# Optimization experiments

Measured on AMD Instinct MI355X. Metric: run time of the kernel, lower is better.

## Reference

```python
import jax, jax.numpy as jnp
import numpy as np

N_NODES = 50000
N_EDGES = 800000
HIDDEN = 128


def setup_inputs() -> dict:
    key = jax.random.key(0)
    ks = jax.random.split(key, 8)
    z = jax.random.normal(ks[0], (N_NODES, HIDDEN), dtype=jnp.float32)
    weights = jax.random.normal(ks[1], (N_EDGES, 1), dtype=jnp.float32)
    sources = jax.random.randint(ks[2], (N_EDGES,), 0, N_NODES)
    dests = jax.random.randint(ks[3], (N_EDGES,), 0, N_NODES)
    # Linear params (stored [in, out]); scale ~ 1/sqrt(fan_in) like torch default
    in_m = 2 * HIDDEN + 1
    in_u = 2 * HIDDEN
    Wm = jax.random.uniform(ks[4], (in_m, HIDDEN), dtype=jnp.float32, minval=-1.0, maxval=1.0) / np.sqrt(in_m)
    bm = jax.random.uniform(ks[5], (HIDDEN,), dtype=jnp.float32, minval=-1.0, maxval=1.0) / np.sqrt(in_m)
    Wu = jax.random.uniform(ks[6], (in_u, HIDDEN), dtype=jnp.float32, minval=-1.0, maxval=1.0) / np.sqrt(in_u)
    bu = jax.random.uniform(ks[7], (HIDDEN,), dtype=jnp.float32, minval=-1.0, maxval=1.0) / np.sqrt(in_u)
    return {"z": z, "weights": weights, "sources": sources, "dests": dests,
            "Wm": Wm, "bm": bm, "Wu": Wu, "bu": bu}


def reference(z, weights, sources, dests, Wm, bm, Wu, bu):
    n = z.shape[0]
    # gather + concat message input: [E, 2d+1]
    inp = jnp.concatenate([z[dests], z[sources], weights], axis=1)
    messages = inp @ Wm + bm                      # [E, d]
    # scatter_reduce amax over destination nodes; empty segments -> -inf
    m = jax.ops.segment_max(messages, dests, num_segments=n)
    m = jnp.where(jnp.isneginf(m), jnp.zeros_like(m), m)
    h = jnp.concatenate([z, m], axis=1) @ Wu + bu  # [N, d]
    return h
```

## Files before the change

kernel.cpp:

```cpp
#include <hip/hip_runtime.h>
#include <math.h>

#define HIDDEN 128
#define PAD_DEG 64
#define NPART 8
#define CHUNK 4096
#define CNT_STRIDE 16
#define NSCATTER_BLOCKS 256
#define XCC_GETREG_IMM 63508

typedef __attribute__((ext_vector_type(8))) _Float16 f16x8;
typedef __attribute__((ext_vector_type(4))) float f32x4;
typedef __attribute__((ext_vector_type(2))) _Float16 h2;

__device__ inline unsigned short f2h(float x) {
    _Float16 h = (_Float16)x;
    return __builtin_bit_cast(unsigned short, h);
}
__device__ inline float h2f(unsigned short u) {
    return (float)__builtin_bit_cast(_Float16, u);
}
__device__ inline float h2f_lo(unsigned int u) { return h2f((unsigned short)(u & 0xffff)); }
__device__ inline float h2f_hi(unsigned int u) { return h2f((unsigned short)(u >> 16)); }
__device__ inline h2 hmax2(h2 a, h2 b) {
    h2 r;
    r[0] = a[0] > b[0] ? a[0] : b[0];
    r[1] = a[1] > b[1] ? a[1] : b[1];
    return r;
}

__global__ void prep_kernel(const float* __restrict__ Wm, const float* __restrict__ Wu,
                            unsigned short* __restrict__ WmT0, unsigned short* __restrict__ WmT1,
                            unsigned short* __restrict__ WuT, float* __restrict__ wlast,
                            int* __restrict__ counts, int* __restrict__ tick, int n) {
    int t = blockIdx.x * blockDim.x + threadIdx.x;
    if (t < 16384) {
        int nn = t >> 7, k = t & 127;
        WmT0[t] = f2h(Wm[k * 128 + nn]);
    } else if (t < 32768) {
        int s = t - 16384;
        int nn = s >> 7, k = s & 127;
        WmT1[s] = f2h(Wm[(128 + k) * 128 + nn]);
    } else if (t < 65536) {
        int s = t - 32768;
        int nn = s >> 8, k = s & 255;
        WuT[s] = f2h(Wu[k * 128 + nn]);
    } else if (t < 65664) {
        int i = t - 65536;
        wlast[i] = Wm[256 * 128 + i];
    } else if (t < 65664 + 4 * n) {
        ((int4*)counts)[t - 65664] = make_int4(0, 0, 0, 0);
    } else if (t < 65664 + 4 * n + 128) {
        tick[t - 65664 - 4 * n] = 0;
    }
}

__global__ __launch_bounds__(256) void fused_sg(const int* __restrict__ dests,
                                                const int* __restrict__ sources,
                                                const float* __restrict__ weights,
                                                int* __restrict__ counts,
                                                int* __restrict__ tick,
                                                unsigned int* __restrict__ edge_pk,
                                                int E, int span, int n, int nchunks,
                                                const float* __restrict__ Z,
                                                const unsigned short* __restrict__ WmT0,
                                                const unsigned short* __restrict__ WmT1,
                                                unsigned short* __restrict__ P1h,
                                                unsigned short* __restrict__ P2h,
                                                int nscatter) {
    __shared__ unsigned short As[64][136];
    __shared__ unsigned short Bs[128][136];
    __shared__ int s_chunk;

    if (blockIdx.x < nscatter) {
        const int xcd = (int)(__builtin_amdgcn_s_getreg(XCC_GETREG_IMM) & 7);
        const int lo = xcd * span;
        const int hi = min(lo + span, n);

        for (int it = 0; it <= nchunks; ++it) {
            if (threadIdx.x == 0) {
                s_chunk = __hip_atomic_fetch_add(&tick[xcd * 16], 1,
                                                 __ATOMIC_RELAXED, __HIP_MEMORY_SCOPE_AGENT);
            }
            __syncthreads();
            const int chunk = s_chunk;
            __syncthreads();
            if (chunk >= nchunks || chunk < 0) break;

            const int base = chunk * CHUNK + threadIdx.x * 4;
            int dd[16];
            unsigned int pk[16];
            int pos[16];

#pragma unroll
            for (int g = 0; g < 4; ++g) {
                int e = base + g * 1024;
                if (e + 3 < E) {
                    int4 dq = *(const int4*)&dests[e];
                    int4 sq = *(const int4*)&sources[e];
                    float4 wq = *(const float4*)&weights[e];
                    dd[g * 4 + 0] = dq.x; dd[g * 4 + 1] = dq.y;
                    dd[g * 4 + 2] = dq.z; dd[g * 4 + 3] = dq.w;
                    pk[g * 4 + 0] = (unsigned int)(sq.x & 0xffff) | ((unsigned int)f2h(wq.x) << 16);
                    pk[g * 4 + 1] = (unsigned int)(sq.y & 0xffff) | ((unsigned int)f2h(wq.y) << 16);
                    pk[g * 4 + 2] = (unsigned int)(sq.z & 0xffff) | ((unsigned int)f2h(wq.z) << 16);
                    pk[g * 4 + 3] = (unsigned int)(sq.w & 0xffff) | ((unsigned int)f2h(wq.w) << 16);
                } else {
#pragma unroll
                    for (int j = 0; j < 4; ++j) {
                        int ej = e + j;
                        if (ej < E) {
                            dd[g * 4 + j] = dests[ej];
                            pk[g * 4 + j] = (unsigned int)(sources[ej] & 0xffff) |
                                            ((unsigned int)f2h(weights[ej]) << 16);
                        } else {
                            dd[g * 4 + j] = -1;
                            pk[g * 4 + j] = 0;
                        }
                    }
                }
            }

#pragma unroll
            for (int k = 0; k < 16; ++k) {
                bool act = (dd[k] >= lo) && (dd[k] < hi);
                pos[k] = act ? atomicAdd(&counts[(size_t)dd[k] * CNT_STRIDE], 1) : PAD_DEG;
            }

#pragma unroll
            for (int k = 0; k < 16; ++k) {
                if (pos[k] < PAD_DEG) {
                    edge_pk[(size_t)dd[k] * PAD_DEG + pos[k]] = pk[k];
                }
            }
        }
        return;
    }

    const int m0 = (blockIdx.x - nscatter) * 64;
    const int tid = threadIdx.x;
    const int wave = tid >> 6, lane = tid & 63;
    const int l15 = lane & 15, q = lane >> 4;
    const int wrow = wave * 16;

#pragma unroll
    for (int i = 0; i < 4; ++i) {
        int f = tid + i * 256;
        int row = f >> 4, c8 = f & 15;
        int gr = min(m0 + row, n - 1);
        const float4* src = (const float4*)&Z[(size_t)gr * 128 + c8 * 8];
        float4 a = src[0], b = src[1];
        f16x8 hv;
        hv[0] = (_Float16)a.x; hv[1] = (_Float16)a.y; hv[2] = (_Float16)a.z; hv[3] = (_Float16)a.w;
        hv[4] = (_Float16)b.x; hv[5] = (_Float16)b.y; hv[6] = (_Float16)b.z; hv[7] = (_Float16)b.w;
        *(f16x8*)&As[row][c8 * 8] = hv;
    }

    for (int part = 0; part < 2; ++part) {
        const float4* bsrc = (const float4*)(part == 0 ? WmT0 : WmT1);
        unsigned short* Out = part == 0 ? P1h : P2h;

#pragma unroll
        for (int i = 0; i < 8; ++i) {
            int f = tid + i * 256;
            int row = f >> 4, c4 = f & 15;
            *(float4*)&Bs[row][c4 * 8] = bsrc[row * 16 + c4];
        }
        __syncthreads();

        f32x4 acc[8];
#pragma unroll
        for (int nt = 0; nt < 8; ++nt) acc[nt] = (f32x4){0.f, 0.f, 0.f, 0.f};

#pragma unroll
        for (int ks = 0; ks < 4; ++ks) {
            int k0 = ks * 32;
            f16x8 a = *(const f16x8*)&As[wrow + l15][k0 + q * 8];
#pragma unroll
            for (int nt = 0; nt < 8; ++nt) {
                f16x8 b = *(const f16x8*)&Bs[nt * 16 + l15][k0 + q * 8];
                acc[nt] = __builtin_amdgcn_mfma_f32_16x16x32_f16(a, b, acc[nt], 0, 0, 0);
            }
        }

#pragma unroll
        for (int nt = 0; nt < 8; ++nt) {
#pragma unroll
            for (int r = 0; r < 4; ++r) {
                int row = m0 + wrow + q * 4 + r;
                if (row < n) Out[(size_t)row * 128 + nt * 16 + l15] = f2h(acc[nt][r]);
            }
        }
        __syncthreads();
    }
}

__global__ __launch_bounds__(256) void segmax_kernel(const unsigned short* __restrict__ P1h,
                                                     const unsigned short* __restrict__ P2h,
                                                     const int* __restrict__ counts,
                                                     const unsigned int* __restrict__ edge_pk,
                                                     const float* __restrict__ wlast,
                                                     const float* __restrict__ bm,
                                                     unsigned short* __restrict__ Mh, int n) {
    const int wave = threadIdx.x >> 6;
    const int lane = threadIdx.x & 63;
    const int v = blockIdx.x * 4 + wave;
    if (v >= n) return;

    const int l16 = lane & 15;
    const int e4 = lane >> 4;
    const uint4* P2q = (const uint4*)P2h;
    const int cnt = min(counts[(size_t)v * CNT_STRIDE], PAD_DEG);

    int pk = (lane < cnt) ? (int)edge_pk[(size_t)v * PAD_DEG + lane] : 0;

    uint4 p1 = make_uint4(0, 0, 0, 0);
    if (e4 == 0 && cnt > 0) p1 = ((const uint4*)P1h)[(size_t)v * 16 + l16];

    float4 wfa = ((const float4*)wlast)[l16 * 2];
    float4 wfb = ((const float4*)wlast)[l16 * 2 + 1];
    h2 wl0, wl1, wl2, wl3;
    wl0[0] = (_Float16)wfa.x; wl0[1] = (_Float16)wfa.y;
    wl1[0] = (_Float16)wfa.z; wl1[1] = (_Float16)wfa.w;
    wl2[0] = (_Float16)wfb.x; wl2[1] = (_Float16)wfb.y;
    wl3[0] = (_Float16)wfb.z; wl3[1] = (_Float16)wfb.w;

    const h2 NEGINF = __builtin_bit_cast(h2, 0xFC00FC00u);
    h2 a0 = NEGINF, a1 = NEGINF, a2 = NEGINF, a3 = NEGINF;

    int j = 0;
    for (; j + 16 <= cnt; j += 16) {
        unsigned int pa = (unsigned int)__shfl(pk, j + e4);
        unsigned int pb = (unsigned int)__shfl(pk, j + 4 + e4);
        unsigned int pc = (unsigned int)__shfl(pk, j + 8 + e4);
        unsigned int pd = (unsigned int)__shfl(pk, j + 12 + e4);
        uint4 ua = P2q[(size_t)(pa & 0xffff) * 16 + l16];
        uint4 ub = P2q[(size_t)(pb & 0xffff) * 16 + l16];
        uint4 uc = P2q[(size_t)(pc & 0xffff) * 16 + l16];
        uint4 ud = P2q[(size_t)(pd & 0xffff) * 16 + l16];
        h2 wva = __builtin_bit_cast(h2, (pa & 0xffff0000u) | (pa >> 16));
        h2 wvb = __builtin_bit_cast(h2, (pb & 0xffff0000u) | (pb >> 16));
        h2 wvc = __builtin_bit_cast(h2, (pc & 0xffff0000u) | (pc >> 16));
        h2 wvd = __builtin_bit_cast(h2, (pd & 0xffff0000u) | (pd >> 16));
        a0 = hmax2(a0, wva * wl0 + __builtin_bit_cast(h2, ua.x));
        a1 = hmax2(a1, wva * wl1 + __builtin_bit_cast(h2, ua.y));
        a2 = hmax2(a2, wva * wl2 + __builtin_bit_cast(h2, ua.z));
        a3 = hmax2(a3, wva * wl3 + __builtin_bit_cast(h2, ua.w));
        a0 = hmax2(a0, wvb * wl0 + __builtin_bit_cast(h2, ub.x));
        a1 = hmax2(a1, wvb * wl1 + __builtin_bit_cast(h2, ub.y));
        a2 = hmax2(a2, wvb * wl2 + __builtin_bit_cast(h2, ub.z));
        a3 = hmax2(a3, wvb * wl3 + __builtin_bit_cast(h2, ub.w));
        a0 = hmax2(a0, wvc * wl0 + __builtin_bit_cast(h2, uc.x));
        a1 = hmax2(a1, wvc * wl1 + __builtin_bit_cast(h2, uc.y));
        a2 = hmax2(a2, wvc * wl2 + __builtin_bit_cast(h2, uc.z));
        a3 = hmax2(a3, wvc * wl3 + __builtin_bit_cast(h2, uc.w));
        a0 = hmax2(a0, wvd * wl0 + __builtin_bit_cast(h2, ud.x));
        a1 = hmax2(a1, wvd * wl1 + __builtin_bit_cast(h2, ud.y));
        a2 = hmax2(a2, wvd * wl2 + __builtin_bit_cast(h2, ud.z));
        a3 = hmax2(a3, wvd * wl3 + __builtin_bit_cast(h2, ud.w));
    }
    for (; j + 8 <= cnt; j += 8) {
        unsigned int pa = (unsigned int)__shfl(pk, j + e4);
        unsigned int pb = (unsigned int)__shfl(pk, j + 4 + e4);
        uint4 ua = P2q[(size_t)(pa & 0xffff) * 16 + l16];
        uint4 ub = P2q[(size_t)(pb & 0xffff) * 16 + l16];
        h2 wva = __builtin_bit_cast(h2, (pa & 0xffff0000u) | (pa >> 16));
        h2 wvb = __builtin_bit_cast(h2, (pb & 0xffff0000u) | (pb >> 16));
        a0 = hmax2(a0, wva * wl0 + __builtin_bit_cast(h2, ua.x));
        a1 = hmax2(a1, wva * wl1 + __builtin_bit_cast(h2, ua.y));
        a2 = hmax2(a2, wva * wl2 + __builtin_bit_cast(h2, ua.z));
        a3 = hmax2(a3, wva * wl3 + __builtin_bit_cast(h2, ua.w));
        a0 = hmax2(a0, wvb * wl0 + __builtin_bit_cast(h2, ub.x));
        a1 = hmax2(a1, wvb * wl1 + __builtin_bit_cast(h2, ub.y));
        a2 = hmax2(a2, wvb * wl2 + __builtin_bit_cast(h2, ub.z));
        a3 = hmax2(a3, wvb * wl3 + __builtin_bit_cast(h2, ub.w));
    }
    for (; j < cnt; j += 4) {
        int idx = j + e4;
        bool valid = idx < cnt;
        unsigned int pa = (unsigned int)__shfl(pk, valid ? idx : 0);
        if (valid) {
            uint4 ua = P2q[(size_t)(pa & 0xffff) * 16 + l16];
            h2 wva = __builtin_bit_cast(h2, (pa & 0xffff0000u) | (pa >> 16));
            a0 = hmax2(a0, wva * wl0 + __builtin_bit_cast(h2, ua.x));
            a1 = hmax2(a1, wva * wl1 + __builtin_bit_cast(h2, ua.y));
            a2 = hmax2(a2, wva * wl2 + __builtin_bit_cast(h2, ua.z));
            a3 = hmax2(a3, wva * wl3 + __builtin_bit_cast(h2, ua.w));
        }
    }

    a0 = hmax2(a0, __builtin_bit_cast(h2, __shfl_xor(__builtin_bit_cast(int, a0), 16)));
    a1 = hmax2(a1, __builtin_bit_cast(h2, __shfl_xor(__builtin_bit_cast(int, a1), 16)));
    a2 = hmax2(a2, __builtin_bit_cast(h2, __shfl_xor(__builtin_bit_cast(int, a2), 16)));
    a3 = hmax2(a3, __builtin_bit_cast(h2, __shfl_xor(__builtin_bit_cast(int, a3), 16)));
    a0 = hmax2(a0, __builtin_bit_cast(h2, __shfl_xor(__builtin_bit_cast(int, a0), 32)));
    a1 = hmax2(a1, __builtin_bit_cast(h2, __shfl_xor(__builtin_bit_cast(int, a1), 32)));
    a2 = hmax2(a2, __builtin_bit_cast(h2, __shfl_xor(__builtin_bit_cast(int, a2), 32)));
    a3 = hmax2(a3, __builtin_bit_cast(h2, __shfl_xor(__builtin_bit_cast(int, a3), 32)));

    if (e4 == 0) {
        uint4 o = make_uint4(0, 0, 0, 0);
        if (cnt > 0) {
            float4 b0 = ((const float4*)bm)[l16 * 2];
            float4 b1 = ((const float4*)bm)[l16 * 2 + 1];
            float m0 = h2f_lo(p1.x) + b0.x + (float)a0[0];
            float m1 = h2f_hi(p1.x) + b0.y + (float)a0[1];
            float m2 = h2f_lo(p1.y) + b0.z + (float)a1[0];
            float m3 = h2f_hi(p1.y) + b0.w + (float)a1[1];
            float m4 = h2f_lo(p1.z) + b1.x + (float)a2[0];
            float m5 = h2f_hi(p1.z) + b1.y + (float)a2[1];
            float m6 = h2f_lo(p1.w) + b1.z + (float)a3[0];
            float m7 = h2f_hi(p1.w) + b1.w + (float)a3[1];
            o.x = (unsigned int)f2h(m0) | ((unsigned int)f2h(m1) << 16);
            o.y = (unsigned int)f2h(m2) | ((unsigned int)f2h(m3) << 16);
            o.z = (unsigned int)f2h(m4) | ((unsigned int)f2h(m5) << 16);
            o.w = (unsigned int)f2h(m6) | ((unsigned int)f2h(m7) << 16);
        } else {
            unsigned int zh = (unsigned int)f2h(0.f);
            unsigned int zz = zh | (zh << 16);
            o = make_uint4(zz, zz, zz, zz);
        }
        ((uint4*)Mh)[(size_t)v * 16 + l16] = o;
    }
}

__global__ __launch_bounds__(256) void gemm_out(const float* __restrict__ Z,
                                                const unsigned short* __restrict__ Mh,
                                                const unsigned short* __restrict__ WuT,
                                                const float* __restrict__ bu,
                                                float* __restrict__ H, int n) {
    __shared__ unsigned short As[64][136];
    __shared__ unsigned short Bs[128][136];

    const int m0 = blockIdx.x * 64;
    const int tid = threadIdx.x;
    const int wave = tid >> 6, lane = tid & 63;
    const int l15 = lane & 15, q = lane >> 4;
    const int wrow = wave * 16;

    f32x4 acc[8];
#pragma unroll
    for (int nt = 0; nt < 8; ++nt) acc[nt] = (f32x4){0.f, 0.f, 0.f, 0.f};

    for (int h = 0; h < 2; ++h) {
#pragma unroll
        for (int i = 0; i < 8; ++i) {
            int f = tid + i * 256;
            int row = f >> 4, c4 = f & 15;
            *(float4*)&Bs[row][c4 * 8] = ((const float4*)WuT)[row * 32 + h * 16 + c4];
        }
        if (h == 0) {
#pragma unroll
            for (int i = 0; i < 4; ++i) {
                int f = tid + i * 256;
                int row = f >> 4, c8 = f & 15;
                int gr = min(m0 + row, n - 1);
                const float4* src = (const float4*)&Z[(size_t)gr * 128 + c8 * 8];
                float4 a = src[0], b = src[1];
                f16x8 hv;
                hv[0] = (_Float16)a.x; hv[1] = (_Float16)a.y; hv[2] = (_Float16)a.z; hv[3] = (_Float16)a.w;
                hv[4] = (_Float16)b.x; hv[5] = (_Float16)b.y; hv[6] = (_Float16)b.z; hv[7] = (_Float16)b.w;
                *(f16x8*)&As[row][c8 * 8] = hv;
            }
        } else {
#pragma unroll
            for (int i = 0; i < 4; ++i) {
                int f = tid + i * 256;
                int row = f >> 4, c4 = f & 15;
                int gr = min(m0 + row, n - 1);
                *(float4*)&As[row][c4 * 8] = ((const float4*)&Mh[(size_t)gr * 128])[c4];
            }
        }
        __syncthreads();

#pragma unroll
        for (int ks = 0; ks < 4; ++ks) {
            int k0 = ks * 32;
            f16x8 a = *(const f16x8*)&As[wrow + l15][k0 + q * 8];
#pragma unroll
            for (int nt = 0; nt < 8; ++nt) {
                f16x8 b = *(const f16x8*)&Bs[nt * 16 + l15][k0 + q * 8];
                acc[nt] = __builtin_amdgcn_mfma_f32_16x16x32_f16(a, b, acc[nt], 0, 0, 0);
            }
        }
        __syncthreads();
    }

#pragma unroll
    for (int nt = 0; nt < 8; ++nt) {
        int col = nt * 16 + l15;
        float bias = bu[col];
#pragma unroll
        for (int r = 0; r < 4; ++r) {
            int row = m0 + wrow + q * 4 + r;
            if (row < n) H[(size_t)row * 128 + col] = acc[nt][r] + bias;
        }
    }
}

extern "C" void kernel_launch(void* const* d_in, const int* in_sizes, int n_in,
                              void* d_out, int out_size, void* d_ws, size_t ws_size,
                              hipStream_t stream) {
    const float* z = (const float*)d_in[0];
    const float* weights = (const float*)d_in[1];
    const int* sources = (const int*)d_in[2];
    const int* dests = (const int*)d_in[3];
    const float* Wm = (const float*)d_in[4];
    const float* bm = (const float*)d_in[5];
    const float* Wu = (const float*)d_in[6];
    const float* bu = (const float*)d_in[7];

    const int n = in_sizes[0] / HIDDEN;
    const int E = in_sizes[1];
    float* H = (float*)d_out;

    char* w = (char*)d_ws;
    auto alloc = [&](size_t bytes) { void* p = w; w += (bytes + 255) & ~(size_t)255; return p; };
    unsigned short* P1h = (unsigned short*)alloc((size_t)n * 128 * 2);
    unsigned short* Mh  = (unsigned short*)alloc((size_t)n * 128 * 2);
    unsigned short* WmT0 = (unsigned short*)alloc(16384 * 2);
    unsigned short* WmT1 = (unsigned short*)alloc(16384 * 2);
    unsigned short* WuT  = (unsigned short*)alloc(32768 * 2);
    float* wlast = (float*)alloc(128 * 4);
    int* counts  = (int*)alloc((size_t)n * CNT_STRIDE * 4);
    int* tick    = (int*)alloc(128 * 4);
    unsigned int* edge_pk = (unsigned int*)alloc((size_t)n * PAD_DEG * 4);

    unsigned short* P2h = (unsigned short*)d_out;

    const int mblocks = (n + 63) / 64;
    const int prep_threads = 65664 + 4 * n + 128;
    const int span = (n + NPART - 1) / NPART;
    const int nchunks = (E + CHUNK - 1) / CHUNK;
    const int nscatter = NSCATTER_BLOCKS;

    prep_kernel<<<(prep_threads + 255) / 256, 256, 0, stream>>>(Wm, Wu, WmT0, WmT1, WuT,
                                                                wlast, counts, tick, n);
    fused_sg<<<nscatter + mblocks, 256, 0, stream>>>(dests, sources, weights, counts, tick,
                                                     edge_pk, E, span, n, nchunks,
                                                     z, WmT0, WmT1, P1h, P2h, nscatter);
    segmax_kernel<<<(n + 3) / 4, 256, 0, stream>>>(P1h, P2h, counts, edge_pk,
                                                   wlast, bm, Mh, n);
    gemm_out<<<mblocks, 256, 0, stream>>>(z, Mh, WuT, bu, H, n);
}
```

Measured before the change: 184.6 us.

## Fuse segment-max into output GEMM, building the message tile in shared memory

Merges the segment-max kernel into the final GEMM. Each wave computes the max-aggregated messages for its 16 rows and writes them straight into the shared-memory A tile, removing the intermediate Mh buffer and one kernel launch. P2h moves from the output buffer to the workspace because the fused kernel writes H while other blocks may still read P2h. The trade-off is much lower parallelism for the latency-bound gather phase: each wave now handles 16 nodes sequentially instead of one, with only a one-node prefetch of edge indices.

```diff
diff --git a/kernel.cpp b/kernel.cpp
--- a/kernel.cpp
+++ b/kernel.cpp
@@ -195,140 +195,16 @@
     }
 }
 
-__global__ __launch_bounds__(256) void segmax_kernel(const unsigned short* __restrict__ P1h,
-                                                     const unsigned short* __restrict__ P2h,
-                                                     const int* __restrict__ counts,
-                                                     const unsigned int* __restrict__ edge_pk,
-                                                     const float* __restrict__ wlast,
-                                                     const float* __restrict__ bm,
-                                                     unsigned short* __restrict__ Mh, int n) {
-    const int wave = threadIdx.x >> 6;
-    const int lane = threadIdx.x & 63;
-    const int v = blockIdx.x * 4 + wave;
-    if (v >= n) return;
-
-    const int l16 = lane & 15;
-    const int e4 = lane >> 4;
-    const uint4* P2q = (const uint4*)P2h;
-    const int cnt = min(counts[(size_t)v * CNT_STRIDE], PAD_DEG);
-
-    int pk = (lane < cnt) ? (int)edge_pk[(size_t)v * PAD_DEG + lane] : 0;
-
-    uint4 p1 = make_uint4(0, 0, 0, 0);
-    if (e4 == 0 && cnt > 0) p1 = ((const uint4*)P1h)[(size_t)v * 16 + l16];
-
-    float4 wfa = ((const float4*)wlast)[l16 * 2];
-    float4 wfb = ((const float4*)wlast)[l16 * 2 + 1];
-    h2 wl0, wl1, wl2, wl3;
-    wl0[0] = (_Float16)wfa.x; wl0[1] = (_Float16)wfa.y;
-    wl1[0] = (_Float16)wfa.z; wl1[1] = (_Float16)wfa.w;
-    wl2[0] = (_Float16)wfb.x; wl2[1] = (_Float16)wfb.y;
-    wl3[0] = (_Float16)wfb.z; wl3[1] = (_Float16)wfb.w;
-
-    const h2 NEGINF = __builtin_bit_cast(h2, 0xFC00FC00u);
-    h2 a0 = NEGINF, a1 = NEGINF, a2 = NEGINF, a3 = NEGINF;
-
-    int j = 0;
-    for (; j + 16 <= cnt; j += 16) {
-        unsigned int pa = (unsigned int)__shfl(pk, j + e4);
-        unsigned int pb = (unsigned int)__shfl(pk, j + 4 + e4);
-        unsigned int pc = (unsigned int)__shfl(pk, j + 8 + e4);
-        unsigned int pd = (unsigned int)__shfl(pk, j + 12 + e4);
-        uint4 ua = P2q[(size_t)(pa & 0xffff) * 16 + l16];
-        uint4 ub = P2q[(size_t)(pb & 0xffff) * 16 + l16];
-        uint4 uc = P2q[(size_t)(pc & 0xffff) * 16 + l16];
-        uint4 ud = P2q[(size_t)(pd & 0xffff) * 16 + l16];
-        h2 wva = __builtin_bit_cast(h2, (pa & 0xffff0000u) | (pa >> 16));
-        h2 wvb = __builtin_bit_cast(h2, (pb & 0xffff0000u) | (pb >> 16));
-        h2 wvc = __builtin_bit_cast(h2, (pc & 0xffff0000u) | (pc >> 16));
-        h2 wvd = __builtin_bit_cast(h2, (pd & 0xffff0000u) | (pd >> 16));
-        a0 = hmax2(a0, wva * wl0 + __builtin_bit_cast(h2, ua.x));
-        a1 = hmax2(a1, wva * wl1 + __builtin_bit_cast(h2, ua.y));
-        a2 = hmax2(a2, wva * wl2 + __builtin_bit_cast(h2, ua.z));
-        a3 = hmax2(a3, wva * wl3 + __builtin_bit_cast(h2, ua.w));
-        a0 = hmax2(a0, wvb * wl0 + __builtin_bit_cast(h2, ub.x));
-        a1 = hmax2(a1, wvb * wl1 + __builtin_bit_cast(h2, ub.y));
-        a2 = hmax2(a2, wvb * wl2 + __builtin_bit_cast(h2, ub.z));
-        a3 = hmax2(a3, wvb * wl3 + __builtin_bit_cast(h2, ub.w));
-        a0 = hmax2(a0, wvc * wl0 + __builtin_bit_cast(h2, uc.x));
-        a1 = hmax2(a1, wvc * wl1 + __builtin_bit_cast(h2, uc.y));
-        a2 = hmax2(a2, wvc * wl2 + __builtin_bit_cast(h2, uc.z));
-        a3 = hmax2(a3, wvc * wl3 + __builtin_bit_cast(h2, uc.w));
-        a0 = hmax2(a0, wvd * wl0 + __builtin_bit_cast(h2, ud.x));
-        a1 = hmax2(a1, wvd * wl1 + __builtin_bit_cast(h2, ud.y));
-        a2 = hmax2(a2, wvd * wl2 + __builtin_bit_cast(h2, ud.z));
-        a3 = hmax2(a3, wvd * wl3 + __builtin_bit_cast(h2, ud.w));
-    }
-    for (; j + 8 <= cnt; j += 8) {
-        unsigned int pa = (unsigned int)__shfl(pk, j + e4);
-        unsigned int pb = (unsigned int)__shfl(pk, j + 4 + e4);
-        uint4 ua = P2q[(size_t)(pa & 0xffff) * 16 + l16];
-        uint4 ub = P2q[(size_t)(pb & 0xffff) * 16 + l16];
-        h2 wva = __builtin_bit_cast(h2, (pa & 0xffff0000u) | (pa >> 16));
-        h2 wvb = __builtin_bit_cast(h2, (pb & 0xffff0000u) | (pb >> 16));
-        a0 = hmax2(a0, wva * wl0 + __builtin_bit_cast(h2, ua.x));
-        a1 = hmax2(a1, wva * wl1 + __builtin_bit_cast(h2, ua.y));
-        a2 = hmax2(a2, wva * wl2 + __builtin_bit_cast(h2, ua.z));
-        a3 = hmax2(a3, wva * wl3 + __builtin_bit_cast(h2, ua.w));
-        a0 = hmax2(a0, wvb * wl0 + __builtin_bit_cast(h2, ub.x));
-        a1 = hmax2(a1, wvb * wl1 + __builtin_bit_cast(h2, ub.y));
-        a2 = hmax2(a2, wvb * wl2 + __builtin_bit_cast(h2, ub.z));
-        a3 = hmax2(a3, wvb * wl3 + __builtin_bit_cast(h2, ub.w));
-    }
-    for (; j < cnt; j += 4) {
-        int idx = j + e4;
-        bool valid = idx < cnt;
-        unsigned int pa = (unsigned int)__shfl(pk, valid ? idx : 0);
-        if (valid) {
-            uint4 ua = P2q[(size_t)(pa & 0xffff) * 16 + l16];
-            h2 wva = __builtin_bit_cast(h2, (pa & 0xffff0000u) | (pa >> 16));
-            a0 = hmax2(a0, wva * wl0 + __builtin_bit_cast(h2, ua.x));
-            a1 = hmax2(a1, wva * wl1 + __builtin_bit_cast(h2, ua.y));
-            a2 = hmax2(a2, wva * wl2 + __builtin_bit_cast(h2, ua.z));
-            a3 = hmax2(a3, wva * wl3 + __builtin_bit_cast(h2, ua.w));
-        }
-    }
-
-    a0 = hmax2(a0, __builtin_bit_cast(h2, __shfl_xor(__builtin_bit_cast(int, a0), 16)));
-    a1 = hmax2(a1, __builtin_bit_cast(h2, __shfl_xor(__builtin_bit_cast(int, a1), 16)));
-    a2 = hmax2(a2, __builtin_bit_cast(h2, __shfl_xor(__builtin_bit_cast(int, a2), 16)));
-    a3 = hmax2(a3, __builtin_bit_cast(h2, __shfl_xor(__builtin_bit_cast(int, a3), 16)));
-    a0 = hmax2(a0, __builtin_bit_cast(h2, __shfl_xor(__builtin_bit_cast(int, a0), 32)));
-    a1 = hmax2(a1, __builtin_bit_cast(h2, __shfl_xor(__builtin_bit_cast(int, a1), 32)));
-    a2 = hmax2(a2, __builtin_bit_cast(h2, __shfl_xor(__builtin_bit_cast(int, a2), 32)));
-    a3 = hmax2(a3, __builtin_bit_cast(h2, __shfl_xor(__builtin_bit_cast(int, a3), 32)));
-
-    if (e4 == 0) {
-        uint4 o = make_uint4(0, 0, 0, 0);
-        if (cnt > 0) {
-            float4 b0 = ((const float4*)bm)[l16 * 2];
-            float4 b1 = ((const float4*)bm)[l16 * 2 + 1];
-            float m0 = h2f_lo(p1.x) + b0.x + (float)a0[0];
-            float m1 = h2f_hi(p1.x) + b0.y + (float)a0[1];
-            float m2 = h2f_lo(p1.y) + b0.z + (float)a1[0];
-            float m3 = h2f_hi(p1.y) + b0.w + (float)a1[1];
-            float m4 = h2f_lo(p1.z) + b1.x + (float)a2[0];
-            float m5 = h2f_hi(p1.z) + b1.y + (float)a2[1];
-            float m6 = h2f_lo(p1.w) + b1.z + (float)a3[0];
-            float m7 = h2f_hi(p1.w) + b1.w + (float)a3[1];
-            o.x = (unsigned int)f2h(m0) | ((unsigned int)f2h(m1) << 16);
-            o.y = (unsigned int)f2h(m2) | ((unsigned int)f2h(m3) << 16);
-            o.z = (unsigned int)f2h(m4) | ((unsigned int)f2h(m5) << 16);
-            o.w = (unsigned int)f2h(m6) | ((unsigned int)f2h(m7) << 16);
-        } else {
-            unsigned int zh = (unsigned int)f2h(0.f);
-            unsigned int zz = zh | (zh << 16);
-            o = make_uint4(zz, zz, zz, zz);
-        }
-        ((uint4*)Mh)[(size_t)v * 16 + l16] = o;
-    }
-}
-
-__global__ __launch_bounds__(256) void gemm_out(const float* __restrict__ Z,
-                                                const unsigned short* __restrict__ Mh,
-                                                const unsigned short* __restrict__ WuT,
-                                                const float* __restrict__ bu,
-                                                float* __restrict__ H, int n) {
+__global__ __launch_bounds__(256) void segmax_gemm(const float* __restrict__ Z,
+                                                   const unsigned short* __restrict__ P1h,
+                                                   const unsigned short* __restrict__ P2h,
+                                                   const int* __restrict__ counts,
+                                                   const unsigned int* __restrict__ edge_pk,
+                                                   const float* __restrict__ wlast,
+                                                   const float* __restrict__ bm,
+                                                   const unsigned short* __restrict__ WuT,
+                                                   const float* __restrict__ bu,
+                                                   float* __restrict__ H, int n) {
     __shared__ unsigned short As[64][136];
     __shared__ unsigned short Bs[128][136];
 
@@ -336,54 +212,195 @@
     const int tid = threadIdx.x;
     const int wave = tid >> 6, lane = tid & 63;
     const int l15 = lane & 15, q = lane >> 4;
+    const int l16 = l15, e4 = q;
     const int wrow = wave * 16;
 
+#pragma unroll
+    for (int i = 0; i < 8; ++i) {
+        int f = tid + i * 256;
+        int row = f >> 4, c4 = f & 15;
+        *(float4*)&Bs[row][c4 * 8] = ((const float4*)WuT)[row * 32 + 16 + c4];
+    }
+
+    {
+        const uint4* P2q = (const uint4*)P2h;
+        const uint4* P1q = (const uint4*)P1h;
+
+        int cntv = 0;
+        {
+            int vvl = m0 + wrow + l16;
+            if (lane < 16 && vvl < n) cntv = min(counts[(size_t)vvl * CNT_STRIDE], PAD_DEG);
+        }
+
+        float4 wfa = ((const float4*)wlast)[l16 * 2];
+        float4 wfb = ((const float4*)wlast)[l16 * 2 + 1];
+        h2 wl0, wl1, wl2, wl3;
+        wl0[0] = (_Float16)wfa.x; wl0[1] = (_Float16)wfa.y;
+        wl1[0] = (_Float16)wfa.z; wl1[1] = (_Float16)wfa.w;
+        wl2[0] = (_Float16)wfb.x; wl2[1] = (_Float16)wfb.y;
+        wl3[0] = (_Float16)wfb.z; wl3[1] = (_Float16)wfb.w;
+        float4 b0 = ((const float4*)bm)[l16 * 2];
+        float4 b1 = ((const float4*)bm)[l16 * 2 + 1];
+
+        const h2 NEGINF = __builtin_bit_cast(h2, 0xFC00FC00u);
+
+        int cnt0 = (m0 + wrow < n) ? __shfl(cntv, 0) : 0;
+        int pk_cur = (lane < cnt0) ? (int)edge_pk[(size_t)(m0 + wrow) * PAD_DEG + lane] : 0;
+
+#pragma unroll 1
+        for (int i = 0; i < 16; ++i) {
+            const int vv = m0 + wrow + i;
+            const int cnt = (vv < n) ? __shfl(cntv, i) : 0;
+
+            int pk_next = 0;
+            if (i < 15) {
+                int vn = vv + 1;
+                int cn = (vn < n) ? __shfl(cntv, i + 1) : 0;
+                pk_next = (lane < cn) ? (int)edge_pk[(size_t)vn * PAD_DEG + lane] : 0;
+            }
+
+            uint4 p1 = make_uint4(0, 0, 0, 0);
+            if (e4 == 0 && cnt > 0) p1 = P1q[(size_t)vv * 16 + l16];
+
+            h2 a0 = NEGINF, a1 = NEGINF, a2 = NEGINF, a3 = NEGINF;
+            int j = 0;
+            for (; j + 16 <= cnt; j += 16) {
+                unsigned int pa = (unsigned int)__shfl(pk_cur, j + e4);
+                unsigned int pb = (unsigned int)__shfl(pk_cur, j + 4 + e4);
+                unsigned int pc = (unsigned int)__shfl(pk_cur, j + 8 + e4);
+                unsigned int pd = (unsigned int)__shfl(pk_cur, j + 12 + e4);
+                uint4 ua = P2q[(size_t)(pa & 0xffff) * 16 + l16];
+                uint4 ub = P2q[(size_t)(pb & 0xffff) * 16 + l16];
+                uint4 uc = P2q[(size_t)(pc & 0xffff) * 16 + l16];
+                uint4 ud = P2q[(size_t)(pd & 0xffff) * 16 + l16];
+                h2 wva = __builtin_bit_cast(h2, (pa & 0xffff0000u) | (pa >> 16));
+                h2 wvb = __builtin_bit_cast(h2, (pb & 0xffff0000u) | (pb >> 16));
+                h2 wvc = __builtin_bit_cast(h2, (pc & 0xffff0000u) | (pc >> 16));
+                h2 wvd = __builtin_bit_cast(h2, (pd & 0xffff0000u) | (pd >> 16));
+                a0 = hmax2(a0, wva * wl0 + __builtin_bit_cast(h2, ua.x));
+                a1 = hmax2(a1, wva * wl1 + __builtin_bit_cast(h2, ua.y));
+                a2 = hmax2(a2, wva * wl2 + __builtin_bit_cast(h2, ua.z));
+                a3 = hmax2(a3, wva * wl3 + __builtin_bit_cast(h2, ua.w));
+                a0 = hmax2(a0, wvb * wl0 + __builtin_bit_cast(h2, ub.x));
+                a1 = hmax2(a1, wvb * wl1 + __builtin_bit_cast(h2, ub.y));
+                a2 = hmax2(a2, wvb * wl2 + __builtin_bit_cast(h2, ub.z));
+                a3 = hmax2(a3, wvb * wl3 + __builtin_bit_cast(h2, ub.w));
+                a0 = hmax2(a0, wvc * wl0 + __builtin_bit_cast(h2, uc.x));
+                a1 = hmax2(a1, wvc * wl1 + __builtin_bit_cast(h2, uc.y));
+                a2 = hmax2(a2, wvc * wl2 + __builtin_bit_cast(h2, uc.z));
+                a3 = hmax2(a3, wvc * wl3 + __builtin_bit_cast(h2, uc.w));
+                a0 = hmax2(a0, wvd * wl0 + __builtin_bit_cast(h2, ud.x));
+                a1 = hmax2(a1, wvd * wl1 + __builtin_bit_cast(h2, ud.y));
+                a2 = hmax2(a2, wvd * wl2 + __builtin_bit_cast(h2, ud.z));
+                a3 = hmax2(a3, wvd * wl3 + __builtin_bit_cast(h2, ud.w));
+            }
+            for (; j + 8 <= cnt; j += 8) {
+                unsigned int pa = (unsigned int)__shfl(pk_cur, j + e4);
+                unsigned int pb = (unsigned int)__shfl(pk_cur, j + 4 + e4);
+                uint4 ua = P2q[(size_t)(pa & 0xffff) * 16 + l16];
+                uint4 ub = P2q[(size_t)(pb & 0xffff) * 16 + l16];
+                h2 wva = __builtin_bit_cast(h2, (pa & 0xffff0000u) | (pa >> 16));
+                h2 wvb = __builtin_bit_cast(h2, (pb & 0xffff0000u) | (pb >> 16));
+                a0 = hmax2(a0, wva * wl0 + __builtin_bit_cast(h2, ua.x));
+                a1 = hmax2(a1, wva * wl1 + __builtin_bit_cast(h2, ua.y));
+                a2 = hmax2(a2, wva * wl2 + __builtin_bit_cast(h2, ua.z));
+                a3 = hmax2(a3, wva * wl3 + __builtin_bit_cast(h2, ua.w));
+                a0 = hmax2(a0, wvb * wl0 + __builtin_bit_cast(h2, ub.x));
+                a1 = hmax2(a1, wvb * wl1 + __builtin_bit_cast(h2, ub.y));
+                a2 = hmax2(a2, wvb * wl2 + __builtin_bit_cast(h2, ub.z));
+                a3 = hmax2(a3, wvb * wl3 + __builtin_bit_cast(h2, ub.w));
+            }
+            for (; j < cnt; j += 4) {
+                int idx = j + e4;
+                bool valid = idx < cnt;
+                unsigned int pa = (unsigned int)__shfl(pk_cur, valid ? idx : 0);
+                if (valid) {
+                    uint4 ua = P2q[(size_t)(pa & 0xffff) * 16 + l16];
+                    h2 wva = __builtin_bit_cast(h2, (pa & 0xffff0000u) | (pa >> 16));
+                    a0 = hmax2(a0, wva * wl0 + __builtin_bit_cast(h2, ua.x));
+                    a1 = hmax2(a1, wva * wl1 + __builtin_bit_cast(h2, ua.y));
+                    a2 = hmax2(a2, wva * wl2 + __builtin_bit_cast(h2, ua.z));
+                    a3 = hmax2(a3, wva * wl3 + __builtin_bit_cast(h2, ua.w));
+                }
+            }
+
+            a0 = hmax2(a0, __builtin_bit_cast(h2, __shfl_xor(__builtin_bit_cast(int, a0), 16)));
+            a1 = hmax2(a1, __builtin_bit_cast(h2, __shfl_xor(__builtin_bit_cast(int, a1), 16)));
+            a2 = hmax2(a2, __builtin_bit_cast(h2, __shfl_xor(__builtin_bit_cast(int, a2), 16)));
+            a3 = hmax2(a3, __builtin_bit_cast(h2, __shfl_xor(__builtin_bit_cast(int, a3), 16)));
+            a0 = hmax2(a0, __builtin_bit_cast(h2, __shfl_xor(__builtin_bit_cast(int, a0), 32)));
+            a1 = hmax2(a1, __builtin_bit_cast(h2, __shfl_xor(__builtin_bit_cast(int, a1), 32)));
+            a2 = hmax2(a2, __builtin_bit_cast(h2, __shfl_xor(__builtin_bit_cast(int, a2), 32)));
+            a3 = hmax2(a3, __builtin_bit_cast(h2, __shfl_xor(__builtin_bit_cast(int, a3), 32)));
+
+            if (e4 == 0) {
+                f16x8 mv;
+                if (cnt > 0) {
+                    mv[0] = (_Float16)(h2f_lo(p1.x) + b0.x + (float)a0[0]);
+                    mv[1] = (_Float16)(h2f_hi(p1.x) + b0.y + (float)a0[1]);
+                    mv[2] = (_Float16)(h2f_lo(p1.y) + b0.z + (float)a1[0]);
+                    mv[3] = (_Float16)(h2f_hi(p1.y) + b0.w + (float)a1[1]);
+                    mv[4] = (_Float16)(h2f_lo(p1.z) + b1.x + (float)a2[0]);
+                    mv[5] = (_Float16)(h2f_hi(p1.z) + b1.y + (float)a2[1]);
+                    mv[6] = (_Float16)(h2f_lo(p1.w) + b1.z + (float)a3[0]);
+                    mv[7] = (_Float16)(h2f_hi(p1.w) + b1.w + (float)a3[1]);
+                } else {
+#pragma unroll
+                    for (int c = 0; c < 8; ++c) mv[c] = (_Float16)0.f;
+                }
+                *(f16x8*)&As[wrow + i][l16 * 8] = mv;
+            }
+
+            pk_cur = pk_next;
+        }
+    }
+    __syncthreads();
+
     f32x4 acc[8];
 #pragma unroll
     for (int nt = 0; nt < 8; ++nt) acc[nt] = (f32x4){0.f, 0.f, 0.f, 0.f};
 
-    for (int h = 0; h < 2; ++h) {
-#pragma unroll
-        for (int i = 0; i < 8; ++i) {
-            int f = tid + i * 256;
-            int row = f >> 4, c4 = f & 15;
-            *(float4*)&Bs[row][c4 * 8] = ((const float4*)WuT)[row * 32 + h * 16 + c4];
-        }
-        if (h == 0) {
-#pragma unroll
-            for (int i = 0; i < 4; ++i) {
-                int f = tid + i * 256;
-                int row = f >> 4, c8 = f & 15;
-                int gr = min(m0 + row, n - 1);
-                const float4* src = (const float4*)&Z[(size_t)gr * 128 + c8 * 8];
-                float4 a = src[0], b = src[1];
-                f16x8 hv;
-                hv[0] = (_Float16)a.x; hv[1] = (_Float16)a.y; hv[2] = (_Float16)a.z; hv[3] = (_Float16)a.w;
-                hv[4] = (_Float16)b.x; hv[5] = (_Float16)b.y; hv[6] = (_Float16)b.z; hv[7] = (_Float16)b.w;
-                *(f16x8*)&As[row][c8 * 8] = hv;
-            }
-        } else {
-#pragma unroll
-            for (int i = 0; i < 4; ++i) {
-                int f = tid + i * 256;
-                int row = f >> 4, c4 = f & 15;
-                int gr = min(m0 + row, n - 1);
-                *(float4*)&As[row][c4 * 8] = ((const float4*)&Mh[(size_t)gr * 128])[c4];
-            }
-        }
-        __syncthreads();
-
-#pragma unroll
-        for (int ks = 0; ks < 4; ++ks) {
-            int k0 = ks * 32;
-            f16x8 a = *(const f16x8*)&As[wrow + l15][k0 + q * 8];
-#pragma unroll
-            for (int nt = 0; nt < 8; ++nt) {
-                f16x8 b = *(const f16x8*)&Bs[nt * 16 + l15][k0 + q * 8];
-                acc[nt] = __builtin_amdgcn_mfma_f32_16x16x32_f16(a, b, acc[nt], 0, 0, 0);
-            }
-        }
-        __syncthreads();
+#pragma unroll
+    for (int ks = 0; ks < 4; ++ks) {
+        int k0 = ks * 32;
+        f16x8 a = *(const f16x8*)&As[wrow + l15][k0 + q * 8];
+#pragma unroll
+        for (int nt = 0; nt < 8; ++nt) {
+            f16x8 b = *(const f16x8*)&Bs[nt * 16 + l15][k0 + q * 8];
+            acc[nt] = __builtin_amdgcn_mfma_f32_16x16x32_f16(a, b, acc[nt], 0, 0, 0);
+        }
+    }
+    __syncthreads();
+
+#pragma unroll
+    for (int i = 0; i < 8; ++i) {
+        int f = tid + i * 256;
+        int row = f >> 4, c4 = f & 15;
+        *(float4*)&Bs[row][c4 * 8] = ((const float4*)WuT)[row * 32 + c4];
+    }
+#pragma unroll
+    for (int i = 0; i < 4; ++i) {
+        int f = tid + i * 256;
+        int row = f >> 4, c8 = f & 15;
+        int gr = min(m0 + row, n - 1);
+        const float4* src = (const float4*)&Z[(size_t)gr * 128 + c8 * 8];
+        float4 a = src[0], b = src[1];
+        f16x8 hv;
+        hv[0] = (_Float16)a.x; hv[1] = (_Float16)a.y; hv[2] = (_Float16)a.z; hv[3] = (_Float16)a.w;
+        hv[4] = (_Float16)b.x; hv[5] = (_Float16)b.y; hv[6] = (_Float16)b.z; hv[7] = (_Float16)b.w;
+        *(f16x8*)&As[row][c8 * 8] = hv;
+    }
+    __syncthreads();
+
+#pragma unroll
+    for (int ks = 0; ks < 4; ++ks) {
+        int k0 = ks * 32;
+        f16x8 a = *(const f16x8*)&As[wrow + l15][k0 + q * 8];
+#pragma unroll
+        for (int nt = 0; nt < 8; ++nt) {
+            f16x8 b = *(const f16x8*)&Bs[nt * 16 + l15][k0 + q * 8];
+            acc[nt] = __builtin_amdgcn_mfma_f32_16x16x32_f16(a, b, acc[nt], 0, 0, 0);
+        }
     }
 
 #pragma unroll
@@ -417,7 +434,7 @@
     char* w = (char*)d_ws;
     auto alloc = [&](size_t bytes) { void* p = w; w += (bytes + 255) & ~(size_t)255; return p; };
     unsigned short* P1h = (unsigned short*)alloc((size_t)n * 128 * 2);
-    unsigned short* Mh  = (unsigned short*)alloc((size_t)n * 128 * 2);
+    unsigned short* P2h = (unsigned short*)alloc((size_t)n * 128 * 2);
     unsigned short* WmT0 = (unsigned short*)alloc(16384 * 2);
     unsigned short* WmT1 = (unsigned short*)alloc(16384 * 2);
     unsigned short* WuT  = (unsigned short*)alloc(32768 * 2);
@@ -426,8 +443,6 @@
     int* tick    = (int*)alloc(128 * 4);
     unsigned int* edge_pk = (unsigned int*)alloc((size_t)n * PAD_DEG * 4);
 
-    unsigned short* P2h = (unsigned short*)d_out;
-
     const int mblocks = (n + 63) / 64;
     const int prep_threads = 65664 + 4 * n + 128;
     const int span = (n + NPART - 1) / NPART;
@@ -439,7 +454,6 @@
     fused_sg<<<nscatter + mblocks, 256, 0, stream>>>(dests, sources, weights, counts, tick,
                                                      edge_pk, E, span, n, nchunks,
                                                      z, WmT0, WmT1, P1h, P2h, nscatter);
-    segmax_kernel<<<(n + 3) / 4, 256, 0, stream>>>(P1h, P2h, counts, edge_pk,
-                                                   wlast, bm, Mh, n);
-    gemm_out<<<mblocks, 256, 0, stream>>>(z, Mh, WuT, bu, H, n);
-}
+    segmax_gemm<<<mblocks, 256, 0, stream>>>(z, P1h, P2h, counts, edge_pk,
+                                             wlast, bm, WuT, bu, H, n);
+}
```

Result: slower. 214.6 us (+16.2%).
